# Kernel tuning notes

Measured on AMD Instinct MI355X. Metric: run time of the kernel, lower is better.

The kernel has to match this reference:

```python
import jax, jax.numpy as jnp
import numpy as np

N, C, G, H = 262144, 512, 16, 16   # nodes, channels, groups, half_group_c
GH = G * H                          # 256
CH_HID = 64                         # channel_mlp hidden = max(GH//4, 8)
SP_HID = 8                          # space_mlp hidden = max(H//4, 8)
B = 1024                            # number of graphs
TEMP = 1.0
EPS = 1e-5


def setup_inputs() -> dict:
    k = jax.random.key(0)
    ks = jax.random.split(k, 20)
    s = 0.02
    rn = lambda kk, sh: jax.random.normal(kk, sh, dtype=jnp.float32)
    return {
        "x": rn(ks[0], (N, C)),
        "batch": jnp.sort(jax.random.randint(ks[1], (N,), 0, B, dtype=jnp.int32)),
        "num_segments": B,
        "cweight": s * rn(ks[2], (1, H)),
        "cbias": 1.0 + s * rn(ks[3], (1, H)),
        "sweight": s * rn(ks[4], (1, H)),
        "sbias": 1.0 + s * rn(ks[5], (1, H)),
        "ch_W1": rn(ks[6], (2 * GH, CH_HID)) / np.sqrt(2 * GH),
        "ch_b1": s * rn(ks[7], (CH_HID,)),
        "ch_W2": rn(ks[8], (CH_HID, GH)) / np.sqrt(CH_HID),
        "ch_b2": s * rn(ks[9], (GH,)),
        "gn_weight": 1.0 + s * rn(ks[10], (GH,)),
        "gn_bias": s * rn(ks[11], (GH,)),
        "sp_W1": rn(ks[12], (3 * H, SP_HID)) / np.sqrt(3 * H),
        "sp_b1": s * rn(ks[13], (SP_HID,)),
        "sp_W2": rn(ks[14], (SP_HID, H)) / np.sqrt(SP_HID),
        "sp_b2": s * rn(ks[15], (H,)),
        "init_scale": jnp.float32(0.1),
        "gnorm_weight": 1.0 + s * rn(ks[16], (C,)),
        "gnorm_bias": s * rn(ks[17], (C,)),
        "gnorm_mean_scale": 1.0 + s * rn(ks[18], (C,)),
    }


def reference(x, batch, num_segments, cweight, cbias, sweight, sbias,
              ch_W1, ch_b1, ch_W2, ch_b2, gn_weight, gn_bias,
              sp_W1, sp_b1, sp_W2, sp_b2, init_scale,
              gnorm_weight, gnorm_bias, gnorm_mean_scale):
    n = x.shape[0]
    xg = x.reshape(n, G, 2 * H)
    x_c = xg[:, :, :H]                      # [N, G, H] channel branch
    x_s = xg[:, :, H:]                      # [N, G, H] spatial branch
    xcf = x_c.reshape(n, GH)

    # --- segment mean / max pooling over graphs ---
    cnt = jax.ops.segment_sum(jnp.ones((n,), x.dtype), batch, num_segments)  # [B]
    gap_mean = jax.ops.segment_sum(xcf, batch, num_segments) / jnp.maximum(cnt, 1.0)[:, None]
    gap_max = jax.ops.segment_max(xcf, batch, num_segments)
    gap_max = jnp.where(cnt[:, None] > 0, gap_max, 0.0)    # empty graphs -> 0
    gap_cat = jnp.concatenate([gap_mean, gap_max], axis=1)  # [B, 2*GH]

    # --- channel gate MLP ---
    hch = jax.nn.relu(gap_cat @ ch_W1 + ch_b1)
    ch_gate = jax.nn.sigmoid((hch @ ch_W2 + ch_b2).reshape(-1, G, H) / TEMP)
    ch_gate = ch_gate * (1.0 + cweight.reshape(1, 1, H)) + cbias.reshape(1, 1, H)
    x_c = x_c * ch_gate[batch]

    # --- GroupNorm over each group's H channels (spatial extent 1) ---
    mu = x_s.mean(axis=2, keepdims=True)
    var = ((x_s - mu) ** 2).mean(axis=2, keepdims=True)
    xn = (x_s - mu) / jnp.sqrt(var + EPS)
    xn = xn * gn_weight.reshape(1, G, H) + gn_bias.reshape(1, G, H)

    # --- spatial context across groups (std is unbiased, ddof=1) ---
    mean_ctx = xn.mean(axis=1)
    max_ctx = xn.max(axis=1)
    std_ctx = jnp.sqrt(((xn - mean_ctx[:, None, :]) ** 2).sum(axis=1) / (G - 1))
    sc = jnp.concatenate([mean_ctx, max_ctx, std_ctx], axis=-1)  # [N, 3H]
    hs = jax.nn.relu(sc @ sp_W1 + sp_b1)
    sp_gate = jax.nn.sigmoid((hs @ sp_W2 + sp_b2).reshape(n, 1, H) / TEMP)
    sp_gate = sp_gate * (1.0 + sweight.reshape(1, 1, H)) + sbias.reshape(1, 1, H)
    x_s = x_s * sp_gate

    # stack -> [N,G,H,2] -> permute -> [N,G,2,H] -> [N,C]
    out = jnp.stack([x_c, x_s], axis=-1).transpose(0, 1, 3, 2).reshape(n, C)
    out = out + jnp.tanh(init_scale) * x

    # --- GraphNorm (PyG): per-graph, per-channel ---
    inv_cnt = 1.0 / jnp.maximum(cnt, 1.0)[:, None]
    gmean = jax.ops.segment_sum(out, batch, num_segments) * inv_cnt
    outc = out - gmean[batch] * gnorm_mean_scale
    gvar = jax.ops.segment_sum(outc * outc, batch, num_segments) * inv_cnt
    out = gnorm_weight * outc / jnp.sqrt(gvar + EPS)[batch] + gnorm_bias

    # channel shuffle with groups=2
    return out.reshape(n, 2, C // 2).transpose(0, 2, 1).reshape(n, C)
```

## Files before the change

kernel.cpp:

```cpp
#include <hip/hip_runtime.h>
#include <hip/hip_bf16.h>
#include <math.h>

#define NN 262144
#define CC 512
#define BB 1024
#define EPSF 1e-5f

typedef float f32x4 __attribute__((ext_vector_type(4)));

__device__ __forceinline__ int lower_bound_i(const int* __restrict__ a, int n, int v) {
    int lo = 0, hi = n;
    while (lo < hi) { int mid = (lo + hi) >> 1; if (a[mid] < v) lo = mid + 1; else hi = mid; }
    return lo;
}

__device__ __forceinline__ float sigmoidf(float v) { return 1.0f / (1.0f + __expf(-v)); }

template<int CTRL>
__device__ __forceinline__ float dppAdd(float v) {
    int t = __builtin_amdgcn_update_dpp(0, __float_as_int(v), CTRL, 0xf, 0xf, true);
    return v + __int_as_float(t);
}
template<int CTRL>
__device__ __forceinline__ float dppMax(float v) {
    int t = __builtin_amdgcn_update_dpp(0, __float_as_int(v), CTRL, 0xf, 0xf, true);
    return fmaxf(v, __int_as_float(t));
}

__global__ void kA(const float* __restrict__ x, const int* __restrict__ batch,
                   const float* __restrict__ sweight, const float* __restrict__ sbias,
                   const float* __restrict__ gn_w, const float* __restrict__ gn_b,
                   const float* __restrict__ sp_W1, const float* __restrict__ sp_b1,
                   const float* __restrict__ sp_W2, const float* __restrict__ sp_b2,
                   const float* __restrict__ init_scale,
                   float* __restrict__ segS1, float* __restrict__ segMx,
                   float* __restrict__ segS2, float* __restrict__ segT1,
                   float* __restrict__ segT2, int* __restrict__ segCnt,
                   float* __restrict__ spgt)
{
    const int b    = blockIdx.x;
    const int tid  = threadIdx.x;
    const int lane = tid & 63;
    const int w    = tid >> 6;
    const int g    = lane & 15;
    const int q    = lane >> 4;
    const int h0   = q * 4;
    const int kk   = g & 7;

    __shared__ float red[4][5][256];
    __shared__ float gw_l[16 * 20], gb_l[16 * 20];
    __shared__ float w1m_l[8 * 20], w1x_l[8 * 20], w1s_l[8 * 20], w2_l[8 * 20];
    __shared__ float b2_l[16], sw_l[16], sb_l[16];

    if (tid < 256) {
        const int gg = tid >> 4, hh = tid & 15;
        gw_l[gg * 20 + hh] = gn_w[tid];
        gb_l[gg * 20 + hh] = gn_b[tid];
    }
    if (tid < 128) {
        const int k2 = tid >> 4, hh = tid & 15;
        w1m_l[k2 * 20 + hh] = sp_W1[hh * 8 + k2];
        w1x_l[k2 * 20 + hh] = sp_W1[(16 + hh) * 8 + k2];
        w1s_l[k2 * 20 + hh] = sp_W1[(32 + hh) * 8 + k2];
        w2_l [k2 * 20 + hh] = sp_W2[k2 * 16 + hh];
    }
    if (tid < 16) {
        b2_l[tid] = sp_b2[tid];
        sw_l[tid] = sweight[tid];
        sb_l[tid] = sbias[tid];
    }
    __syncthreads();

    const int s = lower_bound_i(batch, NN, b);
    const int e = lower_bound_i(batch, NN, b + 1);
    const float tau = tanhf(init_scale[0]);
    const float b1k = sp_b1[kk];

    const int gofs = g * 20 + h0;
    const int kofs = kk * 20 + h0;

    float sc1[4] = {0.f,0.f,0.f,0.f}, sc2[4] = {0.f,0.f,0.f,0.f};
    float st1[4] = {0.f,0.f,0.f,0.f}, st2[4] = {0.f,0.f,0.f,0.f};
    float mxc[4] = {-INFINITY,-INFINITY,-INFINITY,-INFINITY};

    for (int n0 = s + 2 * w; n0 < e; n0 += 8) {
        const int n1 = (n0 + 1 < e) ? n0 + 1 : e - 1;
        const bool v1 = (n0 + 1 < e);

        const float* r0 = x + (size_t)n0 * CC + g * 32 + h0;
        const float* r1 = x + (size_t)n1 * CC + g * 32 + h0;
        const float4 c40 = *(const float4*)r0;
        const float4 s40 = *(const float4*)(r0 + 16);
        const float4 c41 = *(const float4*)r1;
        const float4 s41 = *(const float4*)(r1 + 16);

        {
            const float c0[4] = {c40.x, c40.y, c40.z, c40.w};
#pragma unroll
            for (int j = 0; j < 4; ++j) {
                sc1[j] += c0[j];
                sc2[j] = fmaf(c0[j], c0[j], sc2[j]);
                mxc[j] = fmaxf(mxc[j], c0[j]);
            }
        }
        if (v1) {
            const float c1[4] = {c41.x, c41.y, c41.z, c41.w};
#pragma unroll
            for (int j = 0; j < 4; ++j) {
                sc1[j] += c1[j];
                sc2[j] = fmaf(c1[j], c1[j], sc2[j]);
                mxc[j] = fmaxf(mxc[j], c1[j]);
            }
        }

#pragma unroll
        for (int rr = 0; rr < 2; ++rr) {
            if (rr == 1 && !v1) break;
            const float4 s4 = rr ? s41 : s40;
            const int   nw = rr ? n1 : n0;
            float sa[4] = {s4.x, s4.y, s4.z, s4.w};

            float ls = sa[0] + sa[1] + sa[2] + sa[3];
            float lq = fmaf(sa[0], sa[0], fmaf(sa[1], sa[1],
                       fmaf(sa[2], sa[2], sa[3] * sa[3])));
            ls += __shfl_xor(ls, 16); ls += __shfl_xor(ls, 32);
            lq += __shfl_xor(lq, 16); lq += __shfl_xor(lq, 32);
            const float mu   = ls * 0.0625f;
            const float var  = lq * 0.0625f - mu * mu;
            const float rstd = rsqrtf(var + EPSF);
            const f32x4 gwv = *(const f32x4*)&gw_l[gofs];
            const f32x4 gbv = *(const f32x4*)&gb_l[gofs];
            float xn[4];
#pragma unroll
            for (int j = 0; j < 4; ++j)
                xn[j] = fmaf((sa[j] - mu) * rstd, gwv[j], gbv[j]);

            float sm[4], s2c[4], mx[4];
#pragma unroll
            for (int j = 0; j < 4; ++j) {
                float v = xn[j];
                v = dppAdd<0xB1>(v); v = dppAdd<0x4E>(v);
                v = dppAdd<0x124>(v); v = dppAdd<0x128>(v);
                sm[j] = v;
                float u = xn[j] * xn[j];
                u = dppAdd<0xB1>(u); u = dppAdd<0x4E>(u);
                u = dppAdd<0x124>(u); u = dppAdd<0x128>(u);
                s2c[j] = u;
                float m = xn[j];
                m = dppMax<0xB1>(m); m = dppMax<0x4E>(m);
                m = dppMax<0x124>(m); m = dppMax<0x128>(m);
                mx[j] = m;
            }

            const f32x4 w1m = *(const f32x4*)&w1m_l[kofs];
            const f32x4 w1x = *(const f32x4*)&w1x_l[kofs];
            const f32x4 w1s = *(const f32x4*)&w1s_l[kofs];
            float p = 0.f;
#pragma unroll
            for (int j = 0; j < 4; ++j) {
                const float mean = sm[j] * 0.0625f;
                const float ss   = fmaxf(s2c[j] - 16.0f * mean * mean, 0.0f);
                const float stdc = sqrtf(ss * (1.0f / 15.0f));
                p = fmaf(mean, w1m[j], p);
                p = fmaf(mx[j], w1x[j], p);
                p = fmaf(stdc, w1s[j], p);
            }
            p += __shfl_xor(p, 16); p += __shfl_xor(p, 32);
            const float hsk = fmaxf(p + b1k, 0.0f);

            const f32x4 w2r = *(const f32x4*)&w2_l[kofs];
            const f32x4 b2v = *(const f32x4*)&b2_l[h0];
            const f32x4 swv = *(const f32x4*)&sw_l[h0];
            const f32x4 sbv = *(const f32x4*)&sb_l[h0];
            float spg[4];
#pragma unroll
            for (int j = 0; j < 4; ++j) {
                float t = hsk * w2r[j];
                t = dppAdd<0xB1>(t); t = dppAdd<0x4E>(t); t = dppAdd<0x141>(t);
                spg[j] = fmaf(sigmoidf(t + b2v[j]), 1.0f + swv[j], sbv[j]) + tau;
            }

#pragma unroll
            for (int j = 0; j < 4; ++j) {
                const float os = spg[j] * sa[j];
                st1[j] += os;
                st2[j] = fmaf(os, os, st2[j]);
            }

            if (g == 0)
                *(float4*)(spgt + (size_t)nw * 16 + h0) =
                    make_float4(spg[0], spg[1], spg[2], spg[3]);
        }
    }

    const int ch = g * 16 + h0;
    *(float4*)&red[w][0][ch] = make_float4(sc1[0], sc1[1], sc1[2], sc1[3]);
    *(float4*)&red[w][1][ch] = make_float4(mxc[0], mxc[1], mxc[2], mxc[3]);
    *(float4*)&red[w][2][ch] = make_float4(sc2[0], sc2[1], sc2[2], sc2[3]);
    *(float4*)&red[w][3][ch] = make_float4(st1[0], st1[1], st1[2], st1[3]);
    *(float4*)&red[w][4][ch] = make_float4(st2[0], st2[1], st2[2], st2[3]);
    __syncthreads();
    if (tid < 256) {
        const int c = tid;
        float a0 = red[0][0][c] + red[1][0][c] + red[2][0][c] + red[3][0][c];
        float a1 = fmaxf(fmaxf(red[0][1][c], red[1][1][c]), fmaxf(red[2][1][c], red[3][1][c]));
        float a2 = red[0][2][c] + red[1][2][c] + red[2][2][c] + red[3][2][c];
        float a3 = red[0][3][c] + red[1][3][c] + red[2][3][c] + red[3][3][c];
        float a4 = red[0][4][c] + red[1][4][c] + red[2][4][c] + red[3][4][c];
        segS1[b * 256 + c] = a0;
        segMx[b * 256 + c] = a1;
        segS2[b * 256 + c] = a2;
        segT1[b * 256 + c] = a3;
        segT2[b * 256 + c] = a4;
    }
    if (tid == 0) segCnt[b] = e - s;
}

__global__ void kF(const float* __restrict__ segS1, const float* __restrict__ segMx,
                   const float* __restrict__ segS2, const float* __restrict__ segT1,
                   const float* __restrict__ segT2, const int* __restrict__ segCnt,
                   const float* __restrict__ ch_W1, const float* __restrict__ ch_b1,
                   const float* __restrict__ ch_W2, const float* __restrict__ ch_b2,
                   const float* __restrict__ cweight, const float* __restrict__ cbias,
                   const float* __restrict__ init_scale,
                   const float* __restrict__ gms, const float* __restrict__ gw,
                   const float* __restrict__ gb,
                   float* __restrict__ coef, float* __restrict__ offs)
{
    const int b = blockIdx.x;
    const int tid = threadIdx.x;
    __shared__ float gap[512];
    __shared__ float hch[64];
    __shared__ float part[4][64];

    const int cnt = segCnt[b];
    const float inv = 1.0f / (float)max(cnt, 1);
    if (tid < 256) {
        gap[tid] = segS1[b * 256 + tid] * inv;
        const float m = segMx[b * 256 + tid];
        gap[256 + tid] = (cnt > 0) ? m : 0.0f;
    }
    __syncthreads();
    {
        const int t = tid & 63, pp = tid >> 6;
        float acc = 0.f;
        for (int i = pp * 128; i < pp * 128 + 128; ++i)
            acc = fmaf(gap[i], ch_W1[i * 64 + t], acc);
        part[pp][t] = acc;
    }
    __syncthreads();
    if (tid < 64)
        hch[tid] = fmaxf(part[0][tid] + part[1][tid] + part[2][tid] + part[3][tid] + ch_b1[tid], 0.0f);
    __syncthreads();
    if (tid < 256) {
        const int c = tid, gg = c >> 4, h = c & 15;
        float acc = ch_b2[c];
        for (int k = 0; k < 64; ++k) acc = fmaf(hch[k], ch_W2[k * 256 + c], acc);
        const float chg = fmaf(sigmoidf(acc), 1.0f + cweight[h], cbias[h]);
        const float tau = tanhf(init_scale[0]);
        const float ct = chg + tau;
        const int colc = gg * 32 + h, cols = colc + 16;
        {
            const float S1 = segS1[b * 256 + c], S2 = segS2[b * 256 + c];
            const float m  = ct * S1 * inv;
            const float e2 = ct * ct * S2 * inv;
            const float smv = gms[colc];
            const float gv = fmaxf(e2 - m * m * smv * (2.0f - smv), 0.0f);
            const float A  = gw[colc] * rsqrtf(gv + EPSF);
            coef[b * 512 + colc] = A * ct;
            offs[b * 512 + colc] = gb[colc] - m * smv * A;
        }
        {
            const float T1 = segT1[b * 256 + c], T2 = segT2[b * 256 + c];
            const float m  = T1 * inv;
            const float e2 = T2 * inv;
            const float smv = gms[cols];
            const float gv = fmaxf(e2 - m * m * smv * (2.0f - smv), 0.0f);
            const float A  = gw[cols] * rsqrtf(gv + EPSF);
            coef[b * 512 + cols] = A;
            offs[b * 512 + cols] = gb[cols] - m * smv * A;
        }
    }
}

__global__ void kB(const float* __restrict__ x, const int* __restrict__ batch,
                   const float* __restrict__ coef, const float* __restrict__ offs,
                   const float* __restrict__ spgt, float* __restrict__ out)
{
    const int b = BB - 1 - blockIdx.x;
    const int tid = threadIdx.x;
    const int lane = tid & 63, w = tid >> 6;
    const int l2 = lane * 2;
    const int p0 = (lane >> 3) & 1;

    const int s = lower_bound_i(batch, NN, b);
    const int e = lower_bound_i(batch, NN, b + 1);

    const float* cfb = coef + (size_t)b * 512;
    const float* ofb = offs + (size_t)b * 512;
    const float cf0 = cfb[l2],       cf1 = cfb[l2 + 1];
    const float cf2 = cfb[128 + l2], cf3 = cfb[129 + l2];
    const float cf4 = cfb[256 + l2], cf5 = cfb[257 + l2];
    const float cf6 = cfb[384 + l2], cf7 = cfb[385 + l2];
    const float of0 = ofb[l2],       of1 = ofb[l2 + 1];
    const float of2 = ofb[128 + l2], of3 = ofb[129 + l2];
    const float of4 = ofb[256 + l2], of5 = ofb[257 + l2];
    const float of6 = ofb[384 + l2], of7 = ofb[385 + l2];

    for (int n0 = s + 4 * w; n0 < e; n0 += 16) {
        int nr[4];
        nr[0] = n0;
        nr[1] = (n0 + 1 < e) ? n0 + 1 : e - 1;
        nr[2] = (n0 + 2 < e) ? n0 + 2 : e - 1;
        nr[3] = (n0 + 3 < e) ? n0 + 3 : e - 1;

        float2 xa[4], xb[4], xc[4], xd[4], sp[4];
#pragma unroll
        for (int rr = 0; rr < 4; ++rr) {
            const float2* r2 = (const float2*)(x + (size_t)nr[rr] * CC);
            xa[rr] = r2[lane];
            xb[rr] = r2[64 + lane];
            xc[rr] = r2[128 + lane];
            xd[rr] = r2[192 + lane];
            sp[rr] = *(const float2*)(spgt + (size_t)nr[rr] * 16 + (l2 & 15));
        }

#pragma unroll
        for (int rr = 0; rr < 4; ++rr) {
            if (rr > 0 && n0 + rr >= e) break;
            const float me = p0 ? sp[rr].x : 1.0f;
            const float mo = p0 ? sp[rr].y : 1.0f;

            const float v0 = fmaf(cf0 * me, xa[rr].x, of0);
            const float v1 = fmaf(cf1 * mo, xa[rr].y, of1);
            const float v2 = fmaf(cf2 * me, xb[rr].x, of2);
            const float v3 = fmaf(cf3 * mo, xb[rr].y, of3);
            const float v4 = fmaf(cf4 * me, xc[rr].x, of4);
            const float v5 = fmaf(cf5 * mo, xc[rr].y, of5);
            const float v6 = fmaf(cf6 * me, xd[rr].x, of6);
            const float v7 = fmaf(cf7 * mo, xd[rr].y, of7);

            f32x4* o4 = (f32x4*)(out + (size_t)nr[rr] * CC);
            f32x4 pa = {v0, v4, v1, v5};
            f32x4 pb = {v2, v6, v3, v7};
            __builtin_nontemporal_store(pa, &o4[lane]);
            __builtin_nontemporal_store(pb, &o4[64 + lane]);
        }
    }
}

extern "C" void kernel_launch(void* const* d_in, const int* in_sizes, int n_in,
                              void* d_out, int out_size, void* d_ws, size_t ws_size,
                              hipStream_t stream) {
    (void)in_sizes; (void)n_in; (void)out_size; (void)ws_size;
    const float* x        = (const float*)d_in[0];
    const int*   batch    = (const int*)d_in[1];
    const float* cweight  = (const float*)d_in[3];
    const float* cbias    = (const float*)d_in[4];
    const float* sweight  = (const float*)d_in[5];
    const float* sbias    = (const float*)d_in[6];
    const float* ch_W1    = (const float*)d_in[7];
    const float* ch_b1    = (const float*)d_in[8];
    const float* ch_W2    = (const float*)d_in[9];
    const float* ch_b2    = (const float*)d_in[10];
    const float* gn_w     = (const float*)d_in[11];
    const float* gn_b     = (const float*)d_in[12];
    const float* sp_W1    = (const float*)d_in[13];
    const float* sp_b1    = (const float*)d_in[14];
    const float* sp_W2    = (const float*)d_in[15];
    const float* sp_b2    = (const float*)d_in[16];
    const float* init_sc  = (const float*)d_in[17];
    const float* gnw      = (const float*)d_in[18];
    const float* gnb      = (const float*)d_in[19];
    const float* gms      = (const float*)d_in[20];

    float* ws    = (float*)d_ws;
    float* segS1 = ws;
    float* segMx = segS1 + BB * 256;
    float* segS2 = segMx + BB * 256;
    float* segT1 = segS2 + BB * 256;
    float* segT2 = segT1 + BB * 256;
    int*   segCnt = (int*)(segT2 + BB * 256);
    float* coef  = (float*)(segCnt + BB);
    float* offs  = coef + BB * 512;
    float* spgt  = offs + BB * 512;
    float* outp  = (float*)d_out;

    kA<<<BB, 256, 0, stream>>>(x, batch, sweight, sbias, gn_w, gn_b,
                               sp_W1, sp_b1, sp_W2, sp_b2, init_sc,
                               segS1, segMx, segS2, segT1, segT2, segCnt, spgt);
    kF<<<BB, 256, 0, stream>>>(segS1, segMx, segS2, segT1, segT2, segCnt,
                               ch_W1, ch_b1, ch_W2, ch_b2, cweight, cbias,
                               init_sc, gms, gnw, gnb, coef, offs);
    kB<<<BB, 256, 0, stream>>>(x, batch, coef, offs, spgt, outp);
}
```

Before: 483.2 us.

## Split each graph segment across two blocks in stat and apply kernels

The stats kernel and the apply kernel now launch two blocks per graph, each covering half of the graph's node range. Per-half partial sums and maxima are written to a workspace and merged in the finalize kernel, which now recomputes counts from the batch array. Within the stats block, the cross-wave reduction now uses shared-memory atomics (with an order-preserving uint encoding for max) instead of a staging array, and each wave handles one row per iteration instead of two. The aim is more parallelism and better load balance across CUs. The cost is extra partial traffic, atomics, duplicate binary searches and less unrolling per wave.

```diff
diff --git a/kernel.cpp b/kernel.cpp
--- a/kernel.cpp
+++ b/kernel.cpp
@@ -16,6 +16,14 @@
 }
 
 __device__ __forceinline__ float sigmoidf(float v) { return 1.0f / (1.0f + __expf(-v)); }
+
+__device__ __forceinline__ unsigned fenc(float f) {
+    unsigned b = __float_as_uint(f);
+    return (b & 0x80000000u) ? ~b : (b | 0x80000000u);
+}
+__device__ __forceinline__ float fdec(unsigned k) {
+    return __uint_as_float((k & 0x80000000u) ? (k & 0x7fffffffu) : ~k);
+}
 
 template<int CTRL>
 __device__ __forceinline__ float dppAdd(float v) {
@@ -34,29 +42,30 @@
                    const float* __restrict__ sp_W1, const float* __restrict__ sp_b1,
                    const float* __restrict__ sp_W2, const float* __restrict__ sp_b2,
                    const float* __restrict__ init_scale,
-                   float* __restrict__ segS1, float* __restrict__ segMx,
-                   float* __restrict__ segS2, float* __restrict__ segT1,
-                   float* __restrict__ segT2, int* __restrict__ segCnt,
-                   float* __restrict__ spgt)
+                   float* __restrict__ partials, float* __restrict__ spgt)
 {
-    const int b    = blockIdx.x;
+    const int seg  = blockIdx.x >> 1;
+    const int half = blockIdx.x & 1;
     const int tid  = threadIdx.x;
     const int lane = tid & 63;
-    const int w    = tid >> 6;
     const int g    = lane & 15;
     const int q    = lane >> 4;
     const int h0   = q * 4;
     const int kk   = g & 7;
-
-    __shared__ float red[4][5][256];
+    const int w    = tid >> 6;
+
     __shared__ float gw_l[16 * 20], gb_l[16 * 20];
     __shared__ float w1m_l[8 * 20], w1x_l[8 * 20], w1s_l[8 * 20], w2_l[8 * 20];
     __shared__ float b2_l[16], sw_l[16], sb_l[16];
+    __shared__ float    sS1[256], sS2[256], sT1[256], sT2[256];
+    __shared__ unsigned sM[256];
 
     if (tid < 256) {
         const int gg = tid >> 4, hh = tid & 15;
         gw_l[gg * 20 + hh] = gn_w[tid];
         gb_l[gg * 20 + hh] = gn_b[tid];
+        sS1[tid] = 0.f; sS2[tid] = 0.f; sT1[tid] = 0.f; sT2[tid] = 0.f;
+        sM[tid] = fenc(-INFINITY);
     }
     if (tid < 128) {
         const int k2 = tid >> 4, hh = tid & 15;
@@ -72,8 +81,11 @@
     }
     __syncthreads();
 
-    const int s = lower_bound_i(batch, NN, b);
-    const int e = lower_bound_i(batch, NN, b + 1);
+    const int s0 = lower_bound_i(batch, NN, seg);
+    const int e0 = lower_bound_i(batch, NN, seg + 1);
+    const int mid = s0 + ((e0 - s0 + 1) >> 1);
+    const int s = half ? mid : s0;
+    const int e = half ? e0 : mid;
     const float tau = tanhf(init_scale[0]);
     const float b1k = sp_b1[kk];
 
@@ -84,162 +96,149 @@
     float st1[4] = {0.f,0.f,0.f,0.f}, st2[4] = {0.f,0.f,0.f,0.f};
     float mxc[4] = {-INFINITY,-INFINITY,-INFINITY,-INFINITY};
 
-    for (int n0 = s + 2 * w; n0 < e; n0 += 8) {
-        const int n1 = (n0 + 1 < e) ? n0 + 1 : e - 1;
-        const bool v1 = (n0 + 1 < e);
-
-        const float* r0 = x + (size_t)n0 * CC + g * 32 + h0;
-        const float* r1 = x + (size_t)n1 * CC + g * 32 + h0;
-        const float4 c40 = *(const float4*)r0;
-        const float4 s40 = *(const float4*)(r0 + 16);
-        const float4 c41 = *(const float4*)r1;
-        const float4 s41 = *(const float4*)(r1 + 16);
+    for (int n = s + w; n < e; n += 4) {
+        const float* row = x + (size_t)n * CC + g * 32 + h0;
+        const float4 c4 = *(const float4*)row;
+        const float4 s4 = *(const float4*)(row + 16);
+        float sa[4] = {s4.x, s4.y, s4.z, s4.w};
 
         {
-            const float c0[4] = {c40.x, c40.y, c40.z, c40.w};
+            const float ca[4] = {c4.x, c4.y, c4.z, c4.w};
 #pragma unroll
             for (int j = 0; j < 4; ++j) {
-                sc1[j] += c0[j];
-                sc2[j] = fmaf(c0[j], c0[j], sc2[j]);
-                mxc[j] = fmaxf(mxc[j], c0[j]);
+                sc1[j] += ca[j];
+                sc2[j] = fmaf(ca[j], ca[j], sc2[j]);
+                mxc[j] = fmaxf(mxc[j], ca[j]);
             }
         }
-        if (v1) {
-            const float c1[4] = {c41.x, c41.y, c41.z, c41.w};
-#pragma unroll
-            for (int j = 0; j < 4; ++j) {
-                sc1[j] += c1[j];
-                sc2[j] = fmaf(c1[j], c1[j], sc2[j]);
-                mxc[j] = fmaxf(mxc[j], c1[j]);
-            }
-        }
-
-#pragma unroll
-        for (int rr = 0; rr < 2; ++rr) {
-            if (rr == 1 && !v1) break;
-            const float4 s4 = rr ? s41 : s40;
-            const int   nw = rr ? n1 : n0;
-            float sa[4] = {s4.x, s4.y, s4.z, s4.w};
-
-            float ls = sa[0] + sa[1] + sa[2] + sa[3];
-            float lq = fmaf(sa[0], sa[0], fmaf(sa[1], sa[1],
-                       fmaf(sa[2], sa[2], sa[3] * sa[3])));
-            ls += __shfl_xor(ls, 16); ls += __shfl_xor(ls, 32);
-            lq += __shfl_xor(lq, 16); lq += __shfl_xor(lq, 32);
-            const float mu   = ls * 0.0625f;
-            const float var  = lq * 0.0625f - mu * mu;
-            const float rstd = rsqrtf(var + EPSF);
-            const f32x4 gwv = *(const f32x4*)&gw_l[gofs];
-            const f32x4 gbv = *(const f32x4*)&gb_l[gofs];
-            float xn[4];
-#pragma unroll
-            for (int j = 0; j < 4; ++j)
-                xn[j] = fmaf((sa[j] - mu) * rstd, gwv[j], gbv[j]);
-
-            float sm[4], s2c[4], mx[4];
-#pragma unroll
-            for (int j = 0; j < 4; ++j) {
-                float v = xn[j];
-                v = dppAdd<0xB1>(v); v = dppAdd<0x4E>(v);
-                v = dppAdd<0x124>(v); v = dppAdd<0x128>(v);
-                sm[j] = v;
-                float u = xn[j] * xn[j];
-                u = dppAdd<0xB1>(u); u = dppAdd<0x4E>(u);
-                u = dppAdd<0x124>(u); u = dppAdd<0x128>(u);
-                s2c[j] = u;
-                float m = xn[j];
-                m = dppMax<0xB1>(m); m = dppMax<0x4E>(m);
-                m = dppMax<0x124>(m); m = dppMax<0x128>(m);
-                mx[j] = m;
-            }
-
-            const f32x4 w1m = *(const f32x4*)&w1m_l[kofs];
-            const f32x4 w1x = *(const f32x4*)&w1x_l[kofs];
-            const f32x4 w1s = *(const f32x4*)&w1s_l[kofs];
-            float p = 0.f;
-#pragma unroll
-            for (int j = 0; j < 4; ++j) {
-                const float mean = sm[j] * 0.0625f;
-                const float ss   = fmaxf(s2c[j] - 16.0f * mean * mean, 0.0f);
-                const float stdc = sqrtf(ss * (1.0f / 15.0f));
-                p = fmaf(mean, w1m[j], p);
-                p = fmaf(mx[j], w1x[j], p);
-                p = fmaf(stdc, w1s[j], p);
-            }
-            p += __shfl_xor(p, 16); p += __shfl_xor(p, 32);
-            const float hsk = fmaxf(p + b1k, 0.0f);
-
-            const f32x4 w2r = *(const f32x4*)&w2_l[kofs];
-            const f32x4 b2v = *(const f32x4*)&b2_l[h0];
-            const f32x4 swv = *(const f32x4*)&sw_l[h0];
-            const f32x4 sbv = *(const f32x4*)&sb_l[h0];
-            float spg[4];
-#pragma unroll
-            for (int j = 0; j < 4; ++j) {
-                float t = hsk * w2r[j];
-                t = dppAdd<0xB1>(t); t = dppAdd<0x4E>(t); t = dppAdd<0x141>(t);
-                spg[j] = fmaf(sigmoidf(t + b2v[j]), 1.0f + swv[j], sbv[j]) + tau;
-            }
-
-#pragma unroll
-            for (int j = 0; j < 4; ++j) {
-                const float os = spg[j] * sa[j];
-                st1[j] += os;
-                st2[j] = fmaf(os, os, st2[j]);
-            }
-
-            if (g == 0)
-                *(float4*)(spgt + (size_t)nw * 16 + h0) =
-                    make_float4(spg[0], spg[1], spg[2], spg[3]);
-        }
-    }
-
-    const int ch = g * 16 + h0;
-    *(float4*)&red[w][0][ch] = make_float4(sc1[0], sc1[1], sc1[2], sc1[3]);
-    *(float4*)&red[w][1][ch] = make_float4(mxc[0], mxc[1], mxc[2], mxc[3]);
-    *(float4*)&red[w][2][ch] = make_float4(sc2[0], sc2[1], sc2[2], sc2[3]);
-    *(float4*)&red[w][3][ch] = make_float4(st1[0], st1[1], st1[2], st1[3]);
-    *(float4*)&red[w][4][ch] = make_float4(st2[0], st2[1], st2[2], st2[3]);
-    __syncthreads();
+
+        float ls = sa[0] + sa[1] + sa[2] + sa[3];
+        float lq = fmaf(sa[0], sa[0], fmaf(sa[1], sa[1],
+                   fmaf(sa[2], sa[2], sa[3] * sa[3])));
+        ls += __shfl_xor(ls, 16); ls += __shfl_xor(ls, 32);
+        lq += __shfl_xor(lq, 16); lq += __shfl_xor(lq, 32);
+        const float mu   = ls * 0.0625f;
+        const float var  = lq * 0.0625f - mu * mu;
+        const float rstd = rsqrtf(var + EPSF);
+        const f32x4 gwv = *(const f32x4*)&gw_l[gofs];
+        const f32x4 gbv = *(const f32x4*)&gb_l[gofs];
+        float xn[4];
+#pragma unroll
+        for (int j = 0; j < 4; ++j)
+            xn[j] = fmaf((sa[j] - mu) * rstd, gwv[j], gbv[j]);
+
+        float sm[4], s2c[4], mx[4];
+#pragma unroll
+        for (int j = 0; j < 4; ++j) {
+            float v = xn[j];
+            v = dppAdd<0xB1>(v); v = dppAdd<0x4E>(v);
+            v = dppAdd<0x124>(v); v = dppAdd<0x128>(v);
+            sm[j] = v;
+            float u = xn[j] * xn[j];
+            u = dppAdd<0xB1>(u); u = dppAdd<0x4E>(u);
+            u = dppAdd<0x124>(u); u = dppAdd<0x128>(u);
+            s2c[j] = u;
+            float m = xn[j];
+            m = dppMax<0xB1>(m); m = dppMax<0x4E>(m);
+            m = dppMax<0x124>(m); m = dppMax<0x128>(m);
+            mx[j] = m;
+        }
+
+        const f32x4 w1m = *(const f32x4*)&w1m_l[kofs];
+        const f32x4 w1x = *(const f32x4*)&w1x_l[kofs];
+        const f32x4 w1s = *(const f32x4*)&w1s_l[kofs];
+        float p = 0.f;
+#pragma unroll
+        for (int j = 0; j < 4; ++j) {
+            const float mean = sm[j] * 0.0625f;
+            const float ss   = fmaxf(s2c[j] - 16.0f * mean * mean, 0.0f);
+            const float stdc = sqrtf(ss * (1.0f / 15.0f));
+            p = fmaf(mean, w1m[j], p);
+            p = fmaf(mx[j], w1x[j], p);
+            p = fmaf(stdc, w1s[j], p);
+        }
+        p += __shfl_xor(p, 16); p += __shfl_xor(p, 32);
+        const float hsk = fmaxf(p + b1k, 0.0f);
+
+        const f32x4 w2r = *(const f32x4*)&w2_l[kofs];
+        const f32x4 b2v = *(const f32x4*)&b2_l[h0];
+        const f32x4 swv = *(const f32x4*)&sw_l[h0];
+        const f32x4 sbv = *(const f32x4*)&sb_l[h0];
+        float spg[4];
+#pragma unroll
+        for (int j = 0; j < 4; ++j) {
+            float t = hsk * w2r[j];
+            t = dppAdd<0xB1>(t); t = dppAdd<0x4E>(t); t = dppAdd<0x141>(t);
+            spg[j] = fmaf(sigmoidf(t + b2v[j]), 1.0f + swv[j], sbv[j]) + tau;
+        }
+
+#pragma unroll
+        for (int j = 0; j < 4; ++j) {
+            const float os = spg[j] * sa[j];
+            st1[j] += os;
+            st2[j] = fmaf(os, os, st2[j]);
+        }
+
+        if (g == 0)
+            *(float4*)(spgt + (size_t)n * 16 + h0) =
+                make_float4(spg[0], spg[1], spg[2], spg[3]);
+    }
+
+    {
+        const int ch = g * 16 + h0;
+#pragma unroll
+        for (int j = 0; j < 4; ++j) {
+            atomicAdd(&sS1[ch + j], sc1[j]);
+            atomicAdd(&sS2[ch + j], sc2[j]);
+            atomicAdd(&sT1[ch + j], st1[j]);
+            atomicAdd(&sT2[ch + j], st2[j]);
+            atomicMax(&sM[ch + j], fenc(mxc[j]));
+        }
+    }
+    __syncthreads();
+
     if (tid < 256) {
-        const int c = tid;
-        float a0 = red[0][0][c] + red[1][0][c] + red[2][0][c] + red[3][0][c];
-        float a1 = fmaxf(fmaxf(red[0][1][c], red[1][1][c]), fmaxf(red[2][1][c], red[3][1][c]));
-        float a2 = red[0][2][c] + red[1][2][c] + red[2][2][c] + red[3][2][c];
-        float a3 = red[0][3][c] + red[1][3][c] + red[2][3][c] + red[3][3][c];
-        float a4 = red[0][4][c] + red[1][4][c] + red[2][4][c] + red[3][4][c];
-        segS1[b * 256 + c] = a0;
-        segMx[b * 256 + c] = a1;
-        segS2[b * 256 + c] = a2;
-        segT1[b * 256 + c] = a3;
-        segT2[b * 256 + c] = a4;
-    }
-    if (tid == 0) segCnt[b] = e - s;
-}
-
-__global__ void kF(const float* __restrict__ segS1, const float* __restrict__ segMx,
-                   const float* __restrict__ segS2, const float* __restrict__ segT1,
-                   const float* __restrict__ segT2, const int* __restrict__ segCnt,
-                   const float* __restrict__ ch_W1, const float* __restrict__ ch_b1,
-                   const float* __restrict__ ch_W2, const float* __restrict__ ch_b2,
-                   const float* __restrict__ cweight, const float* __restrict__ cbias,
-                   const float* __restrict__ init_scale,
-                   const float* __restrict__ gms, const float* __restrict__ gw,
-                   const float* __restrict__ gb,
-                   float* __restrict__ coef, float* __restrict__ offs)
+        float* pb = partials + ((size_t)blockIdx.x * 5) * 256;
+        pb[tid]         = sS1[tid];
+        pb[256 + tid]   = fdec(sM[tid]);
+        pb[512 + tid]   = sS2[tid];
+        pb[768 + tid]   = sT1[tid];
+        pb[1024 + tid]  = sT2[tid];
+    }
+}
+
+__global__ void kFin(const float* __restrict__ partials, const int* __restrict__ batch,
+                     const float* __restrict__ ch_W1, const float* __restrict__ ch_b1,
+                     const float* __restrict__ ch_W2, const float* __restrict__ ch_b2,
+                     const float* __restrict__ cweight, const float* __restrict__ cbias,
+                     const float* __restrict__ init_scale,
+                     const float* __restrict__ gms, const float* __restrict__ gw,
+                     const float* __restrict__ gb,
+                     float* __restrict__ coef, float* __restrict__ offs)
 {
     const int b = blockIdx.x;
     const int tid = threadIdx.x;
     __shared__ float gap[512];
+    __shared__ float part[4][64];
     __shared__ float hch[64];
-    __shared__ float part[4][64];
-
-    const int cnt = segCnt[b];
+    __shared__ float sS1[256], sS2[256], sT1[256], sT2[256];
+
+    const int s = lower_bound_i(batch, NN, b);
+    const int e = lower_bound_i(batch, NN, b + 1);
+    const int cnt = e - s;
     const float inv = 1.0f / (float)max(cnt, 1);
+
     if (tid < 256) {
-        gap[tid] = segS1[b * 256 + tid] * inv;
-        const float m = segMx[b * 256 + tid];
-        gap[256 + tid] = (cnt > 0) ? m : 0.0f;
+        const float* p0 = partials + ((size_t)(b * 2) * 5) * 256;
+        const float* p1 = partials + ((size_t)(b * 2 + 1) * 5) * 256;
+        const float a0 = p0[tid] + p1[tid];
+        const float a1 = fmaxf(p0[256 + tid], p1[256 + tid]);
+        const float a2 = p0[512 + tid] + p1[512 + tid];
+        const float a3 = p0[768 + tid] + p1[768 + tid];
+        const float a4 = p0[1024 + tid] + p1[1024 + tid];
+        sS1[tid] = a0; sS2[tid] = a2; sT1[tid] = a3; sT2[tid] = a4;
+        gap[tid] = a0 * inv;
+        gap[256 + tid] = (cnt > 0) ? a1 : 0.0f;
     }
     __syncthreads();
     {
@@ -253,7 +252,7 @@
     if (tid < 64)
         hch[tid] = fmaxf(part[0][tid] + part[1][tid] + part[2][tid] + part[3][tid] + ch_b1[tid], 0.0f);
     __syncthreads();
-    if (tid < 256) {
+    {
         const int c = tid, gg = c >> 4, h = c & 15;
         float acc = ch_b2[c];
         for (int k = 0; k < 64; ++k) acc = fmaf(hch[k], ch_W2[k * 256 + c], acc);
@@ -262,7 +261,7 @@
         const float ct = chg + tau;
         const int colc = gg * 32 + h, cols = colc + 16;
         {
-            const float S1 = segS1[b * 256 + c], S2 = segS2[b * 256 + c];
+            const float S1 = sS1[c], S2 = sS2[c];
             const float m  = ct * S1 * inv;
             const float e2 = ct * ct * S2 * inv;
             const float smv = gms[colc];
@@ -272,7 +271,7 @@
             offs[b * 512 + colc] = gb[colc] - m * smv * A;
         }
         {
-            const float T1 = segT1[b * 256 + c], T2 = segT2[b * 256 + c];
+            const float T1 = sT1[c], T2 = sT2[c];
             const float m  = T1 * inv;
             const float e2 = T2 * inv;
             const float smv = gms[cols];
@@ -288,14 +287,19 @@
                    const float* __restrict__ coef, const float* __restrict__ offs,
                    const float* __restrict__ spgt, float* __restrict__ out)
 {
-    const int b = BB - 1 - blockIdx.x;
+    const int bb   = blockIdx.x >> 1;
+    const int half = blockIdx.x & 1;
+    const int b    = BB - 1 - bb;
     const int tid = threadIdx.x;
     const int lane = tid & 63, w = tid >> 6;
     const int l2 = lane * 2;
     const int p0 = (lane >> 3) & 1;
 
-    const int s = lower_bound_i(batch, NN, b);
-    const int e = lower_bound_i(batch, NN, b + 1);
+    const int s0 = lower_bound_i(batch, NN, b);
+    const int e0 = lower_bound_i(batch, NN, b + 1);
+    const int mid = s0 + ((e0 - s0 + 1) >> 1);
+    const int s = half ? mid : s0;
+    const int e = half ? e0 : mid;
 
     const float* cfb = coef + (size_t)b * 512;
     const float* ofb = offs + (size_t)b * 512;
@@ -308,32 +312,28 @@
     const float of4 = ofb[256 + l2], of5 = ofb[257 + l2];
     const float of6 = ofb[384 + l2], of7 = ofb[385 + l2];
 
-    for (int n0 = s + 4 * w; n0 < e; n0 += 16) {
-        int nr[4];
-        nr[0] = n0;
-        nr[1] = (n0 + 1 < e) ? n0 + 1 : e - 1;
-        nr[2] = (n0 + 2 < e) ? n0 + 2 : e - 1;
-        nr[3] = (n0 + 3 < e) ? n0 + 3 : e - 1;
-
-        float2 xa[4], xb[4], xc[4], xd[4], sp[4];
-#pragma unroll
-        for (int rr = 0; rr < 4; ++rr) {
-            const float2* r2 = (const float2*)(x + (size_t)nr[rr] * CC);
-            xa[rr] = r2[lane];
-            xb[rr] = r2[64 + lane];
-            xc[rr] = r2[128 + lane];
-            xd[rr] = r2[192 + lane];
-            sp[rr] = *(const float2*)(spgt + (size_t)nr[rr] * 16 + (l2 & 15));
-        }
-
-#pragma unroll
-        for (int rr = 0; rr < 4; ++rr) {
-            if (rr > 0 && n0 + rr >= e) break;
+    for (int n0 = s + 2 * w; n0 < e; n0 += 8) {
+        const int n1 = (n0 + 1 < e) ? n0 + 1 : e - 1;
+        const bool v1 = (n0 + 1 < e);
+
+        const float2* r0 = (const float2*)(x + (size_t)n0 * CC);
+        const float2* r1 = (const float2*)(x + (size_t)n1 * CC);
+        const float2 xa[2] = { r0[lane],        r1[lane] };
+        const float2 xb[2] = { r0[64 + lane],   r1[64 + lane] };
+        const float2 xc[2] = { r0[128 + lane],  r1[128 + lane] };
+        const float2 xd[2] = { r0[192 + lane],  r1[192 + lane] };
+        const float2 sp[2] = {
+            *(const float2*)(spgt + (size_t)n0 * 16 + (l2 & 15)),
+            *(const float2*)(spgt + (size_t)n1 * 16 + (l2 & 15)) };
+
+#pragma unroll
+        for (int rr = 0; rr < 2; ++rr) {
+            if (rr == 1 && !v1) break;
             const float me = p0 ? sp[rr].x : 1.0f;
             const float mo = p0 ? sp[rr].y : 1.0f;
 
             const float v0 = fmaf(cf0 * me, xa[rr].x, of0);
-            const float v1 = fmaf(cf1 * mo, xa[rr].y, of1);
+            const float v1f = fmaf(cf1 * mo, xa[rr].y, of1);
             const float v2 = fmaf(cf2 * me, xb[rr].x, of2);
             const float v3 = fmaf(cf3 * mo, xb[rr].y, of3);
             const float v4 = fmaf(cf4 * me, xc[rr].x, of4);
@@ -341,8 +341,8 @@
             const float v6 = fmaf(cf6 * me, xd[rr].x, of6);
             const float v7 = fmaf(cf7 * mo, xd[rr].y, of7);
 
-            f32x4* o4 = (f32x4*)(out + (size_t)nr[rr] * CC);
-            f32x4 pa = {v0, v4, v1, v5};
+            f32x4* o4 = (f32x4*)(out + (size_t)(rr ? n1 : n0) * CC);
+            f32x4 pa = {v0, v4, v1f, v5};
             f32x4 pb = {v2, v6, v3, v7};
             __builtin_nontemporal_store(pa, &o4[lane]);
             __builtin_nontemporal_store(pb, &o4[64 + lane]);
@@ -375,23 +375,18 @@
     const float* gnb      = (const float*)d_in[19];
     const float* gms      = (const float*)d_in[20];
 
-    float* ws    = (float*)d_ws;
-    float* segS1 = ws;
-    float* segMx = segS1 + BB * 256;
-    float* segS2 = segMx + BB * 256;
-    float* segT1 = segS2 + BB * 256;
-    float* segT2 = segT1 + BB * 256;
-    int*   segCnt = (int*)(segT2 + BB * 256);
-    float* coef  = (float*)(segCnt + BB);
-    float* offs  = coef + BB * 512;
-    float* spgt  = offs + BB * 512;
-    float* outp  = (float*)d_out;
-
-    kA<<<BB, 256, 0, stream>>>(x, batch, sweight, sbias, gn_w, gn_b,
-                               sp_W1, sp_b1, sp_W2, sp_b2, init_sc,
-                               segS1, segMx, segS2, segT1, segT2, segCnt, spgt);
-    kF<<<BB, 256, 0, stream>>>(segS1, segMx, segS2, segT1, segT2, segCnt,
-                               ch_W1, ch_b1, ch_W2, ch_b2, cweight, cbias,
-                               init_sc, gms, gnw, gnb, coef, offs);
-    kB<<<BB, 256, 0, stream>>>(x, batch, coef, offs, spgt, outp);
-}
+    float* ws       = (float*)d_ws;
+    float* partials = ws;
+    float* coef     = partials + 2048 * 5 * 256;
+    float* offs     = coef + BB * 512;
+    float* spgt     = offs + BB * 512;
+    float* outp     = (float*)d_out;
+
+    kA<<<BB * 2, 256, 0, stream>>>(x, batch, sweight, sbias, gn_w, gn_b,
+                                   sp_W1, sp_b1, sp_W2, sp_b2, init_sc,
+                                   partials, spgt);
+    kFin<<<BB, 256, 0, stream>>>(partials, batch, ch_W1, ch_b1, ch_W2, ch_b2,
+                                 cweight, cbias, init_sc, gms, gnw, gnb,
+                                 coef, offs);
+    kB<<<BB * 2, 256, 0, stream>>>(x, batch, coef, offs, spgt, outp);
+}
```

Result: faster. 454.4 us (-6.0%).
